# Kernel optimization log

Measured on AMD Instinct MI355X. Metric: run time of the kernel, lower is better.

The kernel has to match this reference:

```python
import jax, jax.numpy as jnp
import numpy as np

N_NODES = 10242
BN_EPS = 1e-5


def _conv(x, idx, w, W, b):
    # x: [N, C]; idx: [N*25*3] int; w: [N, 25, 3]; W: [Cout, 25*C]; b: [Cout]
    n = x.shape[0]
    mat = x[idx].reshape(n, 25, 3, -1)                 # gather: [N,25,3,C]
    agg = jnp.einsum('nkte,nkt->nke', mat, w)          # weighted interp sum over 3 verts
    agg = agg.reshape(n, -1)                           # [N, 25*C]
    return agg @ W.T + b


def _bn_relu(x, g, be):
    # BatchNorm1d in training mode: batch (node-axis) stats, biased variance
    mu = jnp.mean(x, axis=0)
    var = jnp.var(x, axis=0)
    return jax.nn.relu((x - mu) * jax.lax.rsqrt(var + BN_EPS) * g + be)


def setup_inputs() -> dict:
    key = jax.random.key(0)
    ks = jax.random.split(key, 16)
    inp = {}
    inp['x'] = jax.random.normal(ks[0], (N_NODES, 3), dtype=jnp.float32)
    inp['neigh_indices'] = jax.random.randint(ks[1], (N_NODES * 25 * 3,), 0, N_NODES, dtype=jnp.int32)
    w = jax.random.uniform(ks[2], (N_NODES, 25, 3), dtype=jnp.float32)
    inp['neigh_weights'] = w / jnp.sum(w, axis=-1, keepdims=True)  # barycentric-like weights
    def lin(k, cout, cin):
        s = 1.0 / np.sqrt(cin)
        return (jax.random.uniform(k, (cout, cin), dtype=jnp.float32, minval=-s, maxval=s),)
    inp['W1'], = lin(ks[3], 64, 25 * 3);   inp['b1'] = jnp.zeros((64,), jnp.float32)
    inp['g1'] = jnp.ones((64,), jnp.float32);  inp['be1'] = jnp.zeros((64,), jnp.float32)
    inp['W2'], = lin(ks[4], 64, 25 * 64);  inp['b2'] = jnp.zeros((64,), jnp.float32)
    inp['g2'] = jnp.ones((64,), jnp.float32);  inp['be2'] = jnp.zeros((64,), jnp.float32)
    inp['W3'], = lin(ks[5], 128, 25 * 64); inp['b3'] = jnp.zeros((128,), jnp.float32)
    inp['g3'] = jnp.ones((128,), jnp.float32); inp['be3'] = jnp.zeros((128,), jnp.float32)
    inp['Wout'], = lin(ks[6], 36, 25 * 128); inp['bout'] = jnp.zeros((36,), jnp.float32)
    return inp


def reference(x, neigh_indices, neigh_weights, W1, b1, g1, be1, W2, b2, g2, be2,
              W3, b3, g3, be3, Wout, bout):
    h = _bn_relu(_conv(x, neigh_indices, neigh_weights, W1, b1), g1, be1)
    h = _bn_relu(_conv(h, neigh_indices, neigh_weights, W2, b2), g2, be2)
    h = _bn_relu(_conv(h, neigh_indices, neigh_weights, W3, b3), g3, be3)
    out = _conv(h, neigh_indices, neigh_weights, Wout, bout)   # [N, num_classes]
    return out
```

## Files before the change

### kernel.cpp

```cpp
#include <hip/hip_runtime.h>

#define NN 10242

typedef short s8v __attribute__((ext_vector_type(8)));
typedef unsigned int u32x2 __attribute__((ext_vector_type(2)));
typedef float f32x4 __attribute__((ext_vector_type(4)));

static __device__ __forceinline__ float bf2f(unsigned short u) {
    unsigned int i = ((unsigned int)u) << 16;
    return __builtin_bit_cast(float, i);
}
static __device__ __forceinline__ float bfu32lo(unsigned int d) {
    return __builtin_bit_cast(float, d << 16);
}
static __device__ __forceinline__ float bfu32hi(unsigned int d) {
    return __builtin_bit_cast(float, d & 0xffff0000u);
}
static __device__ __forceinline__ unsigned short f2bf(float f) {
    unsigned int i = __builtin_bit_cast(unsigned int, f);
    unsigned int lsb = (i >> 16) & 1u;
    i += 0x7fffu + lsb;
    return (unsigned short)(i >> 16);
}
static __device__ __forceinline__ unsigned int cvtpk(float lo, float hi) {
    unsigned int r;
    asm("v_cvt_pk_bf16_f32 %0, %1, %2" : "=v"(r) : "v"(lo), "v"(hi));
    return r;
}
static __device__ __forceinline__ void gl_lds16(const unsigned short* g, unsigned short* l) {
    __builtin_amdgcn_global_load_lds(
        (const __attribute__((address_space(1))) unsigned int*)g,
        (__attribute__((address_space(3))) unsigned int*)l, 16, 0, 0);
}
template<int N> static __device__ __forceinline__ void waitv() {
    asm volatile("s_waitcnt vmcnt(%0)" :: "n"(N) : "memory");
    __builtin_amdgcn_sched_barrier(0);
}
static __device__ __forceinline__ void lgkm0() {
    asm volatile("s_waitcnt lgkmcnt(0)" ::: "memory");
    __builtin_amdgcn_sched_barrier(0);
}
static __device__ __forceinline__ int imin(int a, int b) { return a < b ? a : b; }

__global__ void detect_k(const void* __restrict__ wgt, int* __restrict__ flag) {
    const float* wf = (const float*)wgt;
    const int r = threadIdx.x;
    float s = wf[3 * r] + wf[3 * r + 1] + wf[3 * r + 2];
    bool ok = (s == s) && (fabsf(s - 1.f) < 0.05f);
    unsigned long long m = __ballot(ok);
    if (r == 0) *flag = (__popcll(m) >= 60) ? 1 : 0;
}

struct Seg { const void* src; void* dst; int n; int nsrc; int mode; int K; int cout; int cpad; };
struct Tab { Seg s[16]; };

__global__ __launch_bounds__(256) void canon_k(Tab t, const int* __restrict__ flag) {
    const Seg sg = t.s[blockIdx.y];
    const bool f32src = (*flag != 0);
    for (int i = blockIdx.x * 256 + threadIdx.x; i < sg.n; i += gridDim.x * 256) {
        if (sg.mode == 0) {
            unsigned short v = 0;
            if (i < sg.nsrc)
                v = f32src ? f2bf(((const float*)sg.src)[i])
                           : ((const unsigned short*)sg.src)[i];
            ((unsigned short*)sg.dst)[i] = v;
        } else if (sg.mode == 1) {
            float v = f32src ? ((const float*)sg.src)[i]
                             : bf2f(((const unsigned short*)sg.src)[i]);
            ((float*)sg.dst)[i] = v;
        } else if (sg.mode == 2) {
            const int row = i / 80, col = i - row * 80;
            unsigned short v = 0;
            if (col < 75) {
                const int j = row * 75 + col;
                v = f32src ? f2bf(((const float*)sg.src)[j])
                           : ((const unsigned short*)sg.src)[j];
            }
            ((unsigned short*)sg.dst)[i] = v;
        } else {
            const int e = i & 7;
            const int r = i >> 3;
            const int c = r % sg.cpad;
            const int k8 = r / sg.cpad;
            unsigned short v = 0;
            if (c < sg.cout) {
                const int j = c * sg.K + k8 * 8 + e;
                v = f32src ? f2bf(((const float*)sg.src)[j])
                           : ((const unsigned short*)sg.src)[j];
            }
            ((unsigned short*)sg.dst)[i] = v;
        }
    }
}

template<int CIN, int COUT, int CG, int NB>
__global__ __launch_bounds__(256) void conv_k(
    const unsigned short* __restrict__ X,
    const int* __restrict__ idx,
    const float* __restrict__ wgt,
    const unsigned short* __restrict__ W,
    const float* __restrict__ bias,
    float* __restrict__ Of)
{
    constexpr int K = 25 * CIN;
    constexpr int KPAD = (K + 7) & ~7;
    __shared__ unsigned short agg[NB][KPAD];
    const int tid = threadIdx.x;
    const int n0 = blockIdx.x * NB;

    for (int p = tid; p < NB * 25; p += 256) {
        const int r = p / 25;
        const int k = p - r * 25;
        const int n = n0 + r;
        if (n < NN) {
            const int base = n * 75 + k * 3;
            const int i0 = idx[base], i1 = idx[base + 1], i2 = idx[base + 2];
            const float w0 = wgt[base], w1 = wgt[base + 1], w2 = wgt[base + 2];
            for (int e = 0; e < CIN; e++) {
                float v = w0 * bf2f(X[i0 * CIN + e]) +
                          w1 * bf2f(X[i1 * CIN + e]) +
                          w2 * bf2f(X[i2 * CIN + e]);
                agg[r][k * CIN + e] = f2bf(v);
            }
        } else {
            for (int e = 0; e < CIN; e++) agg[r][k * CIN + e] = 0;
        }
    }
    if constexpr (KPAD != K) {
        for (int p = tid; p < NB * (KPAD - K); p += 256) {
            const int r = p / (KPAD - K);
            agg[r][K + p - r * (KPAD - K)] = 0;
        }
    }
    __syncthreads();

    constexpr int RG = 256 / CG;
    constexpr int RPT = NB / RG;
    const int c = tid % CG;
    const int rq = tid / CG;
    float acc[RPT] = {};
    if (c < COUT) {
        const unsigned short* Wr = W + (size_t)c * KPAD;
        for (int j = 0; j < KPAD; j += 8) {
            s8v wv = *(const s8v*)(Wr + j);
            float wf[8];
            #pragma unroll
            for (int q = 0; q < 8; q++) wf[q] = bf2f((unsigned short)wv[q]);
            #pragma unroll
            for (int rr = 0; rr < RPT; rr++) {
                s8v av = *(const s8v*)(&agg[rq * RPT + rr][j]);
                #pragma unroll
                for (int q = 0; q < 8; q++)
                    acc[rr] += wf[q] * bf2f((unsigned short)av[q]);
            }
        }
        const float bb = bias[c];
        #pragma unroll
        for (int rr = 0; rr < RPT; rr++) {
            const int n = n0 + rq * RPT + rr;
            if (n < NN) Of[(size_t)n * COUT + c] = acc[rr] + bb;
        }
    }
}

template<int CIN, int COUTP, int COUT, int RING, bool FINAL>
__global__ __launch_bounds__(256, 3) void convdma2_k(
    const unsigned short* __restrict__ X,
    const int* __restrict__ idx,
    const float* __restrict__ wgt,
    const unsigned short* __restrict__ Wt,
    const float* __restrict__ bias,
    float* __restrict__ pre,
    void* __restrict__ Ob,
    const int* __restrict__ flag)
{
    constexpr int NT = CIN / 32;
    constexpr int NFRAG = COUTP / 64;
    constexpr int INSTS = CIN / 8;
    constexpr int Q = INSTS / 4;
    constexpr int R = NT * NFRAG;
    constexpr int UPNS = (CIN == 64) ? 4 : 5;
    constexpr int UNITS = 16 << UPNS;
    __shared__ unsigned short raw[RING * 64 * CIN];
    __shared__ unsigned short agg[2][16][CIN + 8];
    __shared__ int   iL[25 * 64];
    __shared__ float wL[25 * 48];
    const int tid = threadIdx.x;
    const int n0 = blockIdx.x * 16;

    for (int q = tid; q < 16 * 75; q += 256) {
        const int node = q / 75, f = q - node * 75;
        const int k = f / 3, v = f - k * 3;
        const int n = n0 + node;
        const bool ok = n < NN;
        const int g = ok ? (n * 75 + f) : 0;
        iL[k * 64 + node * 4 + v] = ok ? idx[g] : 0;
        wL[k * 48 + node * 3 + v] = ok ? wgt[g] : 0.f;
    }
    for (int q = tid; q < 25 * 16; q += 256)
        iL[(q / 16) * 64 + (q - (q / 16) * 16) * 4 + 3] = 0;
    __syncthreads();

    const int wv = tid >> 6;
    const int lane = tid & 63;
    const int l15 = lane & 15;
    const int kg = lane >> 4;
    const int colbase = wv * NFRAG * 16;

    auto issue = [&](int sd) {
        const int base = (sd & (RING - 1)) * (64 * CIN);
        #pragma unroll
        for (int jj = 0; jj < Q; jj++) {
            const int j = wv * Q + jj;
            int row, p;
            if constexpr (CIN == 64) { row = j * 8 + (lane >> 3); p = lane & 7; }
            else                     { row = j * 4 + (lane >> 4); p = lane & 15; }
            const int id = iL[sd * 64 + row];
            gl_lds16(X + (size_t)id * CIN + p * 8, &raw[base + j * 512]);
        }
    };
    auto loadB = [&](int sp, s8v* dst) {
        #pragma unroll
        for (int t = 0; t < NT; t++)
            #pragma unroll
            for (int j = 0; j < NFRAG; j++)
                dst[t * NFRAG + j] = *(const s8v*)(Wt +
                    ((size_t)(sp * (CIN / 8) + t * 4 + kg) * COUTP + colbase + j * 16 + l15) * 8);
    };

    f32x4 acc[NFRAG] = {};
    s8v breg[2][R];

    if constexpr (RING == 4) { issue(0); issue(1); loadB(0, breg[0]); issue(2); }
    else                     { issue(0); loadB(0, breg[0]); issue(1); }

    #pragma unroll
    for (int s = 0; s < 25; s++) {
        if (s + 1 < 25) loadB(s + 1, breg[(s + 1) & 1]);
        if constexpr (RING == 4) {
            if (s <= 22)      waitv<2 * Q + 2 * R>();
            else if (s == 23) waitv<Q + 2 * R>();
            else              waitv<R>();
        } else {
            if (s <= 23)      waitv<Q + 2 * R>();
            else              waitv<R>();
        }
        __builtin_amdgcn_s_barrier();
        {
            const int sb = (s & (RING - 1)) * (64 * CIN);
            #pragma unroll
            for (int u = tid; u < UNITS; u += 256) {
                const int node = u >> UPNS;
                const int e4 = u & ((1 << UPNS) - 1);
                const float w0 = wL[s * 48 + node * 3 + 0];
                const float w1 = wL[s * 48 + node * 3 + 1];
                const float w2 = wL[s * 48 + node * 3 + 2];
                const int rb = sb + node * 4 * CIN + e4 * 4;
                const u32x2 A = *(const u32x2*)&raw[rb + 0 * CIN];
                const u32x2 B = *(const u32x2*)&raw[rb + 1 * CIN];
                const u32x2 C = *(const u32x2*)&raw[rb + 2 * CIN];
                const float v0 = w0 * bfu32lo(A[0]) + w1 * bfu32lo(B[0]) + w2 * bfu32lo(C[0]);
                const float v1 = w0 * bfu32hi(A[0]) + w1 * bfu32hi(B[0]) + w2 * bfu32hi(C[0]);
                const float v2 = w0 * bfu32lo(A[1]) + w1 * bfu32lo(B[1]) + w2 * bfu32lo(C[1]);
                const float v3 = w0 * bfu32hi(A[1]) + w1 * bfu32hi(B[1]) + w2 * bfu32hi(C[1]);
                u32x2 o;
                o[0] = cvtpk(v0, v1);
                o[1] = cvtpk(v2, v3);
                *(u32x2*)&agg[s & 1][node][e4 * 4] = o;
            }
        }
        if constexpr (RING == 4) { if (s + 3 < 25) issue(s + 3); }
        lgkm0();
        __builtin_amdgcn_s_barrier();
        if constexpr (RING == 2) {
            if (s + 2 < 25) issue(s + 2);
            __builtin_amdgcn_sched_barrier(0);
        }
        #pragma unroll
        for (int t = 0; t < NT; t++) {
            const s8v a = *(const s8v*)(&agg[s & 1][l15][t * 32 + kg * 8]);
            #pragma unroll
            for (int j = 0; j < NFRAG; j++)
                acc[j] = __builtin_amdgcn_mfma_f32_16x16x32_bf16(
                    a, breg[s & 1][t * NFRAG + j], acc[j], 0, 0, 0);
        }
    }

    bool f32o = false;
    if constexpr (FINAL) f32o = (*flag != 0);
    #pragma unroll
    for (int j = 0; j < NFRAG; j++) {
        const int col = colbase + j * 16 + l15;
        if (col < COUT) {
            const float bb = bias[col];
            #pragma unroll
            for (int q = 0; q < 4; q++) {
                const int n = n0 + kg * 4 + q;
                if (n < NN) {
                    const float v = acc[j][q] + bb;
                    if constexpr (FINAL) {
                        if (f32o) ((float*)Ob)[(size_t)n * COUT + col] = v;
                        else ((unsigned short*)Ob)[(size_t)n * COUT + col] = f2bf(v);
                    } else {
                        pre[(size_t)n * COUT + col] = v;
                    }
                }
            }
        }
    }
}

template<int C>
__global__ __launch_bounds__(256) void stats_k(const float* __restrict__ pre,
                                               float* __restrict__ part)
{
    constexpr int RG = 256 / C;
    constexpr int CH = (NN + 63) / 64;
    const int b = blockIdx.x;
    const int r0 = b * CH;
    const int r1 = imin(NN, r0 + CH);
    const int c = threadIdx.x % C;
    const int g = threadIdx.x / C;
    float s = 0.f, s2 = 0.f;
    for (int r = r0 + g; r < r1; r += RG) {
        float v = pre[(size_t)r * C + c];
        s += v; s2 += v * v;
    }
    __shared__ float ls[256], ls2[256];
    ls[threadIdx.x] = s; ls2[threadIdx.x] = s2;
    __syncthreads();
    if (threadIdx.x < C) {
        float a = 0.f, a2 = 0.f;
        #pragma unroll
        for (int g2 = 0; g2 < RG; g2++) {
            a  += ls[g2 * C + threadIdx.x];
            a2 += ls2[g2 * C + threadIdx.x];
        }
        part[b * 2 * C + threadIdx.x] = a;
        part[b * 2 * C + C + threadIdx.x] = a2;
    }
}

template<int C>
__global__ __launch_bounds__(256) void bn_k(const float* __restrict__ pre,
                                            const float* __restrict__ part,
                                            const float* __restrict__ gm,
                                            const float* __restrict__ bt,
                                            unsigned short* __restrict__ act)
{
    __shared__ float sc[C], sh[C];
    if (threadIdx.x < C) {
        const int c = threadIdx.x;
        float s = 0.f, s2 = 0.f;
        for (int b = 0; b < 64; b++) {
            s  += part[b * 2 * C + c];
            s2 += part[b * 2 * C + C + c];
        }
        const float inv = 1.f / (float)NN;
        float mu = s * inv;
        float var = s2 * inv - mu * mu;
        float scale = gm[c] * rsqrtf(var + 1e-5f);
        sc[c] = scale;
        sh[c] = bt[c] - mu * scale;
    }
    __syncthreads();
    const int chunk = (NN + gridDim.x - 1) / gridDim.x;
    const int r0 = blockIdx.x * chunk;
    const int r1 = imin(NN, r0 + chunk);
    for (int i = r0 * C + threadIdx.x; i < r1 * C; i += 256) {
        const int c = i % C;
        float v = fmaxf(pre[i] * sc[c] + sh[c], 0.f);
        act[i] = f2bf(v);
    }
}

extern "C" void kernel_launch(void* const* d_in, const int* in_sizes, int n_in,
                              void* d_out, int out_size, void* d_ws, size_t ws_size,
                              hipStream_t stream) {
    const void* x    = d_in[0];
    const int*  idx  = (const int*)d_in[1];
    const void* wgt  = d_in[2];
    const void* W1   = d_in[3];
    const void* b1   = d_in[4];
    const void* g1   = d_in[5];
    const void* be1  = d_in[6];
    const void* W2   = d_in[7];
    const void* b2   = d_in[8];
    const void* g2   = d_in[9];
    const void* be2  = d_in[10];
    const void* W3   = d_in[11];
    const void* b3   = d_in[12];
    const void* g3   = d_in[13];
    const void* be3  = d_in[14];
    const void* Wout = d_in[15];
    const void* bout = d_in[16];

    char* ws = (char*)d_ws;
    size_t off = 0;
    auto alloc = [&](size_t bytes) {
        off = (off + 255) & ~(size_t)255;
        size_t o = off; off += bytes; return o;
    };
    const size_t o_flag = alloc(4);
    const size_t o_xc   = alloc((size_t)NN * 3 * 2);
    const size_t o_wgtc = alloc((size_t)NN * 75 * 4);
    const size_t o_W1c  = alloc(64 * 80 * 2);
    const size_t o_Wt2  = alloc((size_t)200 * 64 * 8 * 2);
    const size_t o_Wt3  = alloc((size_t)200 * 128 * 8 * 2);
    const size_t o_Wt4  = alloc((size_t)400 * 64 * 8 * 2);
    const size_t o_bias = alloc(1024 * 4);
    const size_t o_pre  = alloc((size_t)NN * 128 * 4);
    const size_t o_actA = alloc((size_t)NN * 128 * 2);
    const size_t o_actB = alloc((size_t)NN * 64 * 2);
    const size_t o_part = alloc((size_t)64 * 2 * 128 * 4);
    if (ws_size < off) return;

    int* flag = (int*)(ws + o_flag);
    unsigned short* xc  = (unsigned short*)(ws + o_xc);
    float* wgtc = (float*)(ws + o_wgtc);
    unsigned short* W1c = (unsigned short*)(ws + o_W1c);
    unsigned short* Wt2 = (unsigned short*)(ws + o_Wt2);
    unsigned short* Wt3 = (unsigned short*)(ws + o_Wt3);
    unsigned short* Wt4 = (unsigned short*)(ws + o_Wt4);
    float* biasc = (float*)(ws + o_bias);
    float* pre  = (float*)(ws + o_pre);
    unsigned short* actA = (unsigned short*)(ws + o_actA);
    unsigned short* actB = (unsigned short*)(ws + o_actB);
    float* part = (float*)(ws + o_part);

    detect_k<<<1, 64, 0, stream>>>(wgt, flag);

    Tab t;
    t.s[0]  = { x,    xc,   NN * 3,         NN * 3,  0, 0, 0, 0 };
    t.s[1]  = { wgt,  wgtc, NN * 75,        NN * 75, 1, 0, 0, 0 };
    t.s[2]  = { W1,   W1c,  64 * 80,        64 * 80, 2, 0, 0, 0 };
    t.s[3]  = { W2,   Wt2,  200 * 64 * 8,   0,       3, 1600, 64, 64 };
    t.s[4]  = { W3,   Wt3,  200 * 128 * 8,  0,       3, 1600, 128, 128 };
    t.s[5]  = { Wout, Wt4,  400 * 64 * 8,   0,       3, 3200, 36, 64 };
    t.s[6]  = { b1,   biasc + 0,   64, 64, 1, 0, 0, 0 };
    t.s[7]  = { g1,   biasc + 64,  64, 64, 1, 0, 0, 0 };
    t.s[8]  = { be1,  biasc + 128, 64, 64, 1, 0, 0, 0 };
    t.s[9]  = { b2,   biasc + 192, 64, 64, 1, 0, 0, 0 };
    t.s[10] = { g2,   biasc + 256, 64, 64, 1, 0, 0, 0 };
    t.s[11] = { be2,  biasc + 320, 64, 64, 1, 0, 0, 0 };
    t.s[12] = { b3,   biasc + 384, 128, 128, 1, 0, 0, 0 };
    t.s[13] = { g3,   biasc + 512, 128, 128, 1, 0, 0, 0 };
    t.s[14] = { be3,  biasc + 640, 128, 128, 1, 0, 0, 0 };
    t.s[15] = { bout, biasc + 768, 36, 36, 1, 0, 0, 0 };
    canon_k<<<dim3(768, 16), 256, 0, stream>>>(t, flag);

    dim3 B(256);
    conv_k<3, 64, 64, 16><<<641, B, 0, stream>>>(xc, idx, wgtc, W1c, biasc + 0, pre);
    stats_k<64><<<64, B, 0, stream>>>(pre, part);
    bn_k<64><<<128, B, 0, stream>>>(pre, part, biasc + 64, biasc + 128, actA);
    convdma2_k<64, 64, 64, 4, false><<<641, B, 0, stream>>>(
        actA, idx, wgtc, Wt2, biasc + 192, pre, nullptr, flag);
    stats_k<64><<<64, B, 0, stream>>>(pre, part);
    bn_k<64><<<128, B, 0, stream>>>(pre, part, biasc + 256, biasc + 320, actB);
    convdma2_k<64, 128, 128, 4, false><<<641, B, 0, stream>>>(
        actB, idx, wgtc, Wt3, biasc + 384, pre, nullptr, flag);
    stats_k<128><<<64, B, 0, stream>>>(pre, part);
    bn_k<128><<<128, B, 0, stream>>>(pre, part, biasc + 512, biasc + 640, actA);
    convdma2_k<128, 64, 36, 2, true><<<641, B, 0, stream>>>(
        actA, idx, wgtc, Wt4, biasc + 768, nullptr, d_out, flag);
}
```

Baseline: 162.5 us.

## Fuse BatchNorm statistics into conv epilogues and pad layer-1 input to four channels

```diff
diff --git a/kernel.cpp b/kernel.cpp
--- a/kernel.cpp
+++ b/kernel.cpp
@@ -77,7 +77,7 @@
                            : ((const unsigned short*)sg.src)[j];
             }
             ((unsigned short*)sg.dst)[i] = v;
-        } else {
+        } else if (sg.mode == 3) {
             const int e = i & 7;
             const int r = i >> 3;
             const int c = r % sg.cpad;
@@ -89,22 +89,33 @@
                            : ((const unsigned short*)sg.src)[j];
             }
             ((unsigned short*)sg.dst)[i] = v;
-        }
-    }
-}
-
-template<int CIN, int COUT, int CG, int NB>
-__global__ __launch_bounds__(256) void conv_k(
-    const unsigned short* __restrict__ X,
+        } else {
+            const int row = i >> 2, col = i & 3;
+            unsigned short v = 0;
+            if (col < 3) {
+                const int j = row * 3 + col;
+                v = f32src ? f2bf(((const float*)sg.src)[j])
+                           : ((const unsigned short*)sg.src)[j];
+            }
+            ((unsigned short*)sg.dst)[i] = v;
+        }
+    }
+}
+
+template<int CIN4, int COUT, int CG, int NB>
+__global__ __launch_bounds__(256) void conv1_k(
+    const unsigned short* __restrict__ X4,
     const int* __restrict__ idx,
     const float* __restrict__ wgt,
     const unsigned short* __restrict__ W,
     const float* __restrict__ bias,
-    float* __restrict__ Of)
+    float* __restrict__ Of,
+    float* __restrict__ part)
 {
-    constexpr int K = 25 * CIN;
-    constexpr int KPAD = (K + 7) & ~7;
+    constexpr int K = 75;
+    constexpr int KPAD = 80;
     __shared__ unsigned short agg[NB][KPAD];
+    __shared__ float ls[256], ls2[256];
     const int tid = threadIdx.x;
     const int n0 = blockIdx.x * NB;
 
@@ -116,21 +127,24 @@
             const int base = n * 75 + k * 3;
             const int i0 = idx[base], i1 = idx[base + 1], i2 = idx[base + 2];
             const float w0 = wgt[base], w1 = wgt[base + 1], w2 = wgt[base + 2];
-            for (int e = 0; e < CIN; e++) {
-                float v = w0 * bf2f(X[i0 * CIN + e]) +
-                          w1 * bf2f(X[i1 * CIN + e]) +
-                          w2 * bf2f(X[i2 * CIN + e]);
-                agg[r][k * CIN + e] = f2bf(v);
+            const unsigned long long A = *(const unsigned long long*)(X4 + (size_t)i0 * 4);
+            const unsigned long long B = *(const unsigned long long*)(X4 + (size_t)i1 * 4);
+            const unsigned long long C = *(const unsigned long long*)(X4 + (size_t)i2 * 4);
+            #pragma unroll
+            for (int e = 0; e < 3; e++) {
+                float v = w0 * bf2f((unsigned short)(A >> (16 * e))) +
+                          w1 * bf2f((unsigned short)(B >> (16 * e))) +
+                          w2 * bf2f((unsigned short)(C >> (16 * e)));
+                agg[r][k * 3 + e] = f2bf(v);
             }
         } else {
-            for (int e = 0; e < CIN; e++) agg[r][k * CIN + e] = 0;
-        }
-    }
-    if constexpr (KPAD != K) {
-        for (int p = tid; p < NB * (KPAD - K); p += 256) {
-            const int r = p / (KPAD - K);
-            agg[r][K + p - r * (KPAD - K)] = 0;
-        }
+            #pragma unroll
+            for (int e = 0; e < 3; e++) agg[r][k * 3 + e] = 0;
+        }
+    }
+    for (int p = tid; p < NB * (KPAD - K); p += 256) {
+        const int r = p / (KPAD - K);
+        agg[r][K + p - r * (KPAD - K)] = 0;
     }
     __syncthreads();
 
@@ -139,27 +153,42 @@
     const int c = tid % CG;
     const int rq = tid / CG;
     float acc[RPT] = {};
-    if (c < COUT) {
-        const unsigned short* Wr = W + (size_t)c * KPAD;
-        for (int j = 0; j < KPAD; j += 8) {
-            s8v wv = *(const s8v*)(Wr + j);
-            float wf[8];
-            #pragma unroll
-            for (int q = 0; q < 8; q++) wf[q] = bf2f((unsigned short)wv[q]);
-            #pragma unroll
-            for (int rr = 0; rr < RPT; rr++) {
-                s8v av = *(const s8v*)(&agg[rq * RPT + rr][j]);
-                #pragma unroll
-                for (int q = 0; q < 8; q++)
-                    acc[rr] += wf[q] * bf2f((unsigned short)av[q]);
-            }
-        }
-        const float bb = bias[c];
+    const unsigned short* Wr = W + (size_t)c * KPAD;
+    for (int j = 0; j < KPAD; j += 8) {
+        s8v wv = *(const s8v*)(Wr + j);
+        float wf[8];
+        #pragma unroll
+        for (int q = 0; q < 8; q++) wf[q] = bf2f((unsigned short)wv[q]);
         #pragma unroll
         for (int rr = 0; rr < RPT; rr++) {
-            const int n = n0 + rq * RPT + rr;
-            if (n < NN) Of[(size_t)n * COUT + c] = acc[rr] + bb;
-        }
+            s8v av = *(const s8v*)(&agg[rq * RPT + rr][j]);
+            #pragma unroll
+            for (int q = 0; q < 8; q++)
+                acc[rr] += wf[q] * bf2f((unsigned short)av[q]);
+        }
+    }
+    const float bb = bias[c];
+    float s = 0.f, s2 = 0.f;
+    #pragma unroll
+    for (int rr = 0; rr < RPT; rr++) {
+        const int n = n0 + rq * RPT + rr;
+        if (n < NN) {
+            const float v = acc[rr] + bb;
+            Of[(size_t)n * COUT + c] = v;
+            s += v; s2 += v * v;
+        }
+    }
+    ls[tid] = s; ls2[tid] = s2;
+    __syncthreads();
+    if (tid < COUT) {
+        float a = 0.f, a2 = 0.f;
+        #pragma unroll
+        for (int g2 = 0; g2 < RG; g2++) {
+            a  += ls[g2 * CG + tid];
+            a2 += ls2[g2 * CG + tid];
+        }
+        part[(size_t)blockIdx.x * 2 * COUT + tid] = a;
+        part[(size_t)blockIdx.x * 2 * COUT + COUT + tid] = a2;
     }
 }
 
@@ -172,7 +201,8 @@
     const float* __restrict__ bias,
     float* __restrict__ pre,
     void* __restrict__ Ob,
-    const int* __restrict__ flag)
+    const int* __restrict__ flag,
+    float* __restrict__ part)
 {
     constexpr int NT = CIN / 32;
     constexpr int NFRAG = COUTP / 64;
@@ -291,6 +321,7 @@
     #pragma unroll
     for (int j = 0; j < NFRAG; j++) {
         const int col = colbase + j * 16 + l15;
+        float s = 0.f, s2 = 0.f;
         if (col < COUT) {
             const float bb = bias[col];
             #pragma unroll
@@ -303,45 +334,23 @@
                         else ((unsigned short*)Ob)[(size_t)n * COUT + col] = f2bf(v);
                     } else {
                         pre[(size_t)n * COUT + col] = v;
+                        s += v; s2 += v * v;
                     }
                 }
             }
         }
-    }
-}
-
-template<int C>
-__global__ __launch_bounds__(256) void stats_k(const float* __restrict__ pre,
-                                               float* __restrict__ part)
-{
-    constexpr int RG = 256 / C;
-    constexpr int CH = (NN + 63) / 64;
-    const int b = blockIdx.x;
-    const int r0 = b * CH;
-    const int r1 = imin(NN, r0 + CH);
-    const int c = threadIdx.x % C;
-    const int g = threadIdx.x / C;
-    float s = 0.f, s2 = 0.f;
-    for (int r = r0 + g; r < r1; r += RG) {
-        float v = pre[(size_t)r * C + c];
-        s += v; s2 += v * v;
-    }
-    __shared__ float ls[256], ls2[256];
-    ls[threadIdx.x] = s; ls2[threadIdx.x] = s2;
-    __syncthreads();
-    if (threadIdx.x < C) {
-        float a = 0.f, a2 = 0.f;
-        #pragma unroll
-        for (int g2 = 0; g2 < RG; g2++) {
-            a  += ls[g2 * C + threadIdx.x];
-            a2 += ls2[g2 * C + threadIdx.x];
-        }
-        part[b * 2 * C + threadIdx.x] = a;
-        part[b * 2 * C + C + threadIdx.x] = a2;
-    }
-}
-
-template<int C>
+        if constexpr (!FINAL) {
+            s  += __shfl_xor(s, 16);  s  += __shfl_xor(s, 32);
+            s2 += __shfl_xor(s2, 16); s2 += __shfl_xor(s2, 32);
+            if (kg == 0) {
+                part[(size_t)blockIdx.x * 2 * COUT + col] = s;
+                part[(size_t)blockIdx.x * 2 * COUT + COUT + col] = s2;
+            }
+        }
+    }
+}
+
+template<int C, int NBLK>
 __global__ __launch_bounds__(256) void bn_k(const float* __restrict__ pre,
                                             const float* __restrict__ part,
                                             const float* __restrict__ gm,
@@ -349,27 +358,38 @@
                                             unsigned short* __restrict__ act)
 {
     __shared__ float sc[C], sh[C];
+    __shared__ float ls[256], ls2[256];
+    constexpr int RG = 256 / C;
+    const int c = threadIdx.x % C;
+    const int g = threadIdx.x / C;
+    float s = 0.f, s2 = 0.f;
+    for (int b = g; b < NBLK; b += RG) {
+        s  += part[(size_t)b * 2 * C + c];
+        s2 += part[(size_t)b * 2 * C + C + c];
+    }
+    ls[threadIdx.x] = s; ls2[threadIdx.x] = s2;
+    __syncthreads();
     if (threadIdx.x < C) {
-        const int c = threadIdx.x;
-        float s = 0.f, s2 = 0.f;
-        for (int b = 0; b < 64; b++) {
-            s  += part[b * 2 * C + c];
-            s2 += part[b * 2 * C + C + c];
+        float a = 0.f, a2 = 0.f;
+        #pragma unroll
+        for (int g2 = 0; g2 < RG; g2++) {
+            a  += ls[g2 * C + threadIdx.x];
+            a2 += ls2[g2 * C + threadIdx.x];
         }
         const float inv = 1.f / (float)NN;
-        float mu = s * inv;
-        float var = s2 * inv - mu * mu;
-        float scale = gm[c] * rsqrtf(var + 1e-5f);
-        sc[c] = scale;
-        sh[c] = bt[c] - mu * scale;
+        float mu = a * inv;
+        float var = a2 * inv - mu * mu;
+        float scale = gm[threadIdx.x] * rsqrtf(var + 1e-5f);
+        sc[threadIdx.x] = scale;
+        sh[threadIdx.x] = bt[threadIdx.x] - mu * scale;
     }
     __syncthreads();
     const int chunk = (NN + gridDim.x - 1) / gridDim.x;
     const int r0 = blockIdx.x * chunk;
     const int r1 = imin(NN, r0 + chunk);
     for (int i = r0 * C + threadIdx.x; i < r1 * C; i += 256) {
-        const int c = i % C;
-        float v = fmaxf(pre[i] * sc[c] + sh[c], 0.f);
+        const int c2 = i % C;
+        float v = fmaxf(pre[i] * sc[c2] + sh[c2], 0.f);
         act[i] = f2bf(v);
     }
 }
@@ -402,7 +422,7 @@
         size_t o = off; off += bytes; return o;
     };
     const size_t o_flag = alloc(4);
-    const size_t o_xc   = alloc((size_t)NN * 3 * 2);
+    const size_t o_x4   = alloc((size_t)NN * 4 * 2);
     const size_t o_wgtc = alloc((size_t)NN * 75 * 4);
     const size_t o_W1c  = alloc(64 * 80 * 2);
     const size_t o_Wt2  = alloc((size_t)200 * 64 * 8 * 2);
@@ -412,11 +432,11 @@
     const size_t o_pre  = alloc((size_t)NN * 128 * 4);
     const size_t o_actA = alloc((size_t)NN * 128 * 2);
     const size_t o_actB = alloc((size_t)NN * 64 * 2);
-    const size_t o_part = alloc((size_t)64 * 2 * 128 * 4);
+    const size_t o_part = alloc((size_t)641 * 2 * 128 * 4);
     if (ws_size < off) return;
 
     int* flag = (int*)(ws + o_flag);
-    unsigned short* xc  = (unsigned short*)(ws + o_xc);
+    unsigned short* x4  = (unsigned short*)(ws + o_x4);
     float* wgtc = (float*)(ws + o_wgtc);
     unsigned short* W1c = (unsigned short*)(ws + o_W1c);
     unsigned short* Wt2 = (unsigned short*)(ws + o_Wt2);
@@ -431,7 +451,7 @@
     detect_k<<<1, 64, 0, stream>>>(wgt, flag);
 
     Tab t;
-    t.s[0]  = { x,    xc,   NN * 3,         NN * 3,  0, 0, 0, 0 };
+    t.s[0]  = { x,    x4,   NN * 4,         NN * 3,  4, 0, 0, 0 };
     t.s[1]  = { wgt,  wgtc, NN * 75,        NN * 75, 1, 0, 0, 0 };
     t.s[2]  = { W1,   W1c,  64 * 80,        64 * 80, 2, 0, 0, 0 };
     t.s[3]  = { W2,   Wt2,  200 * 64 * 8,   0,       3, 1600, 64, 64 };
@@ -450,17 +470,14 @@
     canon_k<<<dim3(768, 16), 256, 0, stream>>>(t, flag);
 
     dim3 B(256);
-    conv_k<3, 64, 64, 16><<<641, B, 0, stream>>>(xc, idx, wgtc, W1c, biasc + 0, pre);
-    stats_k<64><<<64, B, 0, stream>>>(pre, part);
-    bn_k<64><<<128, B, 0, stream>>>(pre, part, biasc + 64, biasc + 128, actA);
+    conv1_k<4, 64, 64, 16><<<641, B, 0, stream>>>(x4, idx, wgtc, W1c, biasc + 0, pre, part);
+    bn_k<64, 641><<<128, B, 0, stream>>>(pre, part, biasc + 64, biasc + 128, actA);
     convdma2_k<64, 64, 64, 4, false><<<641, B, 0, stream>>>(
-        actA, idx, wgtc, Wt2, biasc + 192, pre, nullptr, flag);
-    stats_k<64><<<64, B, 0, stream>>>(pre, part);
-    bn_k<64><<<128, B, 0, stream>>>(pre, part, biasc + 256, biasc + 320, actB);
+        actA, idx, wgtc, Wt2, biasc + 192, pre, nullptr, flag, part);
+    bn_k<64, 641><<<128, B, 0, stream>>>(pre, part, biasc + 256, biasc + 320, actB);
     convdma2_k<64, 128, 128, 4, false><<<641, B, 0, stream>>>(
-        actB, idx, wgtc, Wt3, biasc + 384, pre, nullptr, flag);
-    stats_k<128><<<64, B, 0, stream>>>(pre, part);
-    bn_k<128><<<128, B, 0, stream>>>(pre, part, biasc + 512, biasc + 640, actA);
+        actB, idx, wgtc, Wt3, biasc + 384, pre, nullptr, flag, part);
+    bn_k<128, 641><<<128, B, 0, stream>>>(pre, part, biasc + 512, biasc + 640, actA);
     convdma2_k<128, 64, 36, 2, true><<<641, B, 0, stream>>>(
-        actA, idx, wgtc, Wt4, biasc + 768, nullptr, d_out, flag);
-}
+        actA, idx, wgtc, Wt4, biasc + 768, nullptr, d_out, flag, nullptr);
+}
```

After: 268.1 us. 1.65x slower.
